# Performance work log

Measured on AMD Instinct MI355X. Metric: run time of the kernel, lower is better.

Reference implementation:

```python
import jax, jax.numpy as jnp
import numpy as np

N_IN = 200000   # input points/voxels
N_OUT = 100000  # output points (downconv transition)
E = 1600000     # neighbor-list entries (edges)
K = 9           # kernel_size: number of spatial filter bins
C_IN = 32
C_A = 24        # unnormalized branch channels (output_channels - normalized_channels)
C_B = 8         # importance-normalized branch channels


def setup_inputs() -> dict:
    key = jax.random.key(0)
    ks = jax.random.split(key, 8)
    feats = jax.random.normal(ks[0], (N_IN, C_IN), dtype=jnp.float32)
    importance = jax.random.uniform(ks[1], (N_IN,), dtype=jnp.float32)
    W_a = jax.random.normal(ks[2], (K, C_IN, C_A), dtype=jnp.float32) * 0.05
    b_a = jnp.zeros((C_A,), dtype=jnp.float32)
    W_b = jax.random.normal(ks[3], (K, C_IN, C_B), dtype=jnp.float32) * 0.05
    b_b = jnp.zeros((C_B,), dtype=jnp.float32)
    neighbors_index = jax.random.randint(ks[4], (E,), 0, N_IN, dtype=jnp.int32)
    neighbors_kernel_index = jax.random.randint(ks[5], (E,), 0, K, dtype=jnp.int32)
    neighbors_out_index = jnp.sort(jax.random.randint(ks[6], (E,), 0, N_OUT, dtype=jnp.int32))
    return {
        'feats': feats, 'importance': importance,
        'W_a': W_a, 'b_a': b_a, 'W_b': W_b, 'b_b': b_b,
        'neighbors_index': neighbors_index,
        'neighbors_kernel_index': neighbors_kernel_index,
        'neighbors_out_index': neighbors_out_index,
    }


def reference(feats, importance, W_a, b_a, W_b, b_b,
              neighbors_index, neighbors_kernel_index, neighbors_out_index):
    # Gather input features along the neighbor list: [E, C_IN]
    gathered = feats[neighbors_index]
    # Combined segment id = output point * K + kernel bin, so one segment_sum
    # accumulates per-(output-point, kernel-bin) feature sums: [N_OUT, K, C_IN]
    seg = neighbors_out_index * K + neighbors_kernel_index

    # --- conv1a: plain sparse conv (no normalization) ---
    Sa = jax.ops.segment_sum(gathered, seg, num_segments=N_OUT * K)
    Sa = Sa.reshape(N_OUT, K, C_IN)
    feats_a = jax.nn.relu(jnp.einsum('nkc,kcf->nf', Sa, W_a) + b_a)

    # --- conv1b: importance-weighted, normalized sparse conv ---
    imp_e = importance[neighbors_index]  # per-edge importance from input points
    Sb = jax.ops.segment_sum(gathered * imp_e[:, None], seg, num_segments=N_OUT * K)
    Sb = Sb.reshape(N_OUT, K, C_IN)
    out_imp = jax.ops.segment_sum(imp_e, neighbors_out_index, num_segments=N_OUT)
    denom = jnp.where(out_imp > 0, out_imp, 1.0)
    feats_b = jax.nn.relu(jnp.einsum('nkc,kcf->nf', Sb, W_b) / denom[:, None] + b_b)

    feats1 = jnp.concatenate([feats_a, feats_b], axis=-1)  # [N_OUT, C_A + C_B]
    return feats1, out_imp
```

## Files before the change

kernel.cpp:

```cpp
#include <hip/hip_runtime.h>
#include <hip/hip_bf16.h>

static constexpr int KC   = 9;
static constexpr int CIN  = 32;
static constexpr int CA   = 24;
static constexpr int CB   = 8;
static constexpr int COUT = 32;
static constexpr int KCC  = KC * CIN;
static constexpr int SPP  = 2 * KCC;

__global__ void prep(const int* __restrict__ oidx, const int* __restrict__ nidx,
                     const float* __restrict__ importance,
                     const float* __restrict__ Wa, const float* __restrict__ Wb,
                     int* __restrict__ rp, float* __restrict__ imp_e,
                     float* __restrict__ Wc, int E, int nout) {
    int e = blockIdx.x * blockDim.x + threadIdx.x;
    if (e < E) {
        int cur  = oidx[e];
        int prev = (e == 0) ? -1 : oidx[e - 1];
        for (int id = prev + 1; id <= cur; ++id) rp[id] = e;
        if (e == E - 1) {
            for (int id = cur + 1; id <= nout; ++id) rp[id] = E;
        }
        imp_e[e] = importance[nidx[e]];
        if (e < KCC * COUT) {
            int f  = e & (COUT - 1);
            int kc = e >> 5;
            Wc[e] = (f < CA) ? Wa[kc * CA + f] : Wb[kc * CB + (f - CA)];
        }
    }
}

#define ACC_ADD(Q, V)                              \
    do {                                           \
        if      ((Q) == 0) acc[0] += (V);          \
        else if ((Q) == 1) acc[1] += (V);          \
        else if ((Q) == 2) acc[2] += (V);          \
        else if ((Q) == 3) acc[3] += (V);          \
        else if ((Q) == 4) acc[4] += (V);          \
        else if ((Q) == 5) acc[5] += (V);          \
        else if ((Q) == 6) acc[6] += (V);          \
        else if ((Q) == 7) acc[7] += (V);          \
        else               acc[8] += (V);          \
    } while (0)

__device__ __forceinline__ float readlane_f(float v, int l) {
    return __uint_as_float(__builtin_amdgcn_readlane(__float_as_uint(v), l));
}

__global__ __launch_bounds__(256) void accum_y(
    const float* __restrict__ feats, const float* __restrict__ imp_e,
    const int* __restrict__ nidx, const int* __restrict__ nkidx,
    const int* __restrict__ rp,
    __hip_bfloat16* __restrict__ S, float* __restrict__ impAcc, int nout)
{
    const int lane = threadIdx.x & 63;
    const int c    = lane & 31;
    const int h    = lane >> 5;
    const int l4   = lane & 3;
    int gw = (blockIdx.x * 256 + threadIdx.x) >> 6;
    gw = __builtin_amdgcn_readfirstlane(gw);
    const int NW = (gridDim.x * 256) >> 6;

    for (int n = gw; n < nout; n += NW) {
        const int start = rp[n];
        const int end   = rp[n + 1];

        float acc[KC];
#pragma unroll
        for (int k = 0; k < KC; ++k) acc[k] = 0.f;
        float accImp = 0.f;

        for (int e = start; e < end; e += 4) {
            int em = e + l4;
            if (em > end - 1) em = end - 1;
            int   metaI = nidx[em];
            int   metaQ = nkidx[em];
            float metaM = imp_e[em];

            int q0 = __builtin_amdgcn_readlane(metaQ, 0);
            int q1 = __builtin_amdgcn_readlane(metaQ, 1);
            int q2 = __builtin_amdgcn_readlane(metaQ, 2);
            int q3 = __builtin_amdgcn_readlane(metaQ, 3);
            int i0 = __builtin_amdgcn_readlane(metaI, 0);
            int i1 = __builtin_amdgcn_readlane(metaI, 1);
            int i2 = __builtin_amdgcn_readlane(metaI, 2);
            int i3 = __builtin_amdgcn_readlane(metaI, 3);
            float m0 = readlane_f(metaM, 0);
            float m1 = readlane_f(metaM, 1);
            float m2 = readlane_f(metaM, 2);
            float m3 = readlane_f(metaM, 3);

            float f0 = feats[(size_t)i0 * CIN + c];
            float f1 = feats[(size_t)i1 * CIN + c];
            float f2 = feats[(size_t)i2 * CIN + c];
            float f3 = feats[(size_t)i3 * CIN + c];

            if (e + 1 >= end) { f1 = 0.f; m1 = 0.f; }
            if (e + 2 >= end) { f2 = 0.f; m2 = 0.f; }
            if (e + 3 >= end) { f3 = 0.f; m3 = 0.f; }
            accImp += (m0 + m1) + (m2 + m3);

            float v0 = f0 * (h ? m0 : 1.0f);
            float v1 = f1 * (h ? m1 : 1.0f);
            float v2 = f2 * (h ? m2 : 1.0f);
            float v3 = f3 * (h ? m3 : 1.0f);
            ACC_ADD(q0, v0);
            ACC_ADD(q1, v1);
            ACC_ADD(q2, v2);
            ACC_ADD(q3, v3);
        }

        __hip_bfloat16* Sp = S + (size_t)n * SPP + h * KCC + c;
#pragma unroll
        for (int k = 0; k < KC; ++k) Sp[k * CIN] = __float2bfloat16(acc[k]);
        if (lane == 0) impAcc[n] = accImp;
    }
}
#undef ACC_ADD

__global__ __launch_bounds__(256) void epilogue_g(
    const __hip_bfloat16* __restrict__ S, const float* __restrict__ impAcc,
    const float* __restrict__ Wc, const float* __restrict__ ba,
    const float* __restrict__ bb,
    float* __restrict__ outf, float* __restrict__ outimp, int nout)
{
    const int gtid   = blockIdx.x * 256 + threadIdx.x;
    const bool valid = (gtid < nout);
    const int n      = valid ? gtid : (nout - 1);

    const unsigned short* Sp =
        reinterpret_cast<const unsigned short*>(S + (size_t)n * SPP);

    float acc[COUT];
#pragma unroll
    for (int j = 0; j < COUT; ++j) acc[j] = 0.f;

    for (int t = 0; t < KCC; t += 8) {
        uint4 ua = *reinterpret_cast<const uint4*>(Sp + t);
        uint4 ub = *reinterpret_cast<const uint4*>(Sp + KCC + t);
        unsigned int uaw[4] = {ua.x, ua.y, ua.z, ua.w};
        unsigned int ubw[4] = {ub.x, ub.y, ub.z, ub.w};
        float sav[8], sbv[8];
#pragma unroll
        for (int p = 0; p < 4; ++p) {
            sav[2 * p]     = __uint_as_float(uaw[p] << 16);
            sav[2 * p + 1] = __uint_as_float(uaw[p] & 0xffff0000u);
            sbv[2 * p]     = __uint_as_float(ubw[p] << 16);
            sbv[2 * p + 1] = __uint_as_float(ubw[p] & 0xffff0000u);
        }
#pragma unroll
        for (int u = 0; u < 8; ++u) {
            const float* w = Wc + (t + u) * COUT;
#pragma unroll
            for (int j = 0; j < CA; ++j) acc[j] = fmaf(sav[u], w[j], acc[j]);
#pragma unroll
            for (int j = 0; j < CB; ++j)
                acc[CA + j] = fmaf(sbv[u], w[CA + j], acc[CA + j]);
        }
    }

    float impTot = impAcc[n];
    float denom  = impTot > 0.f ? impTot : 1.f;

    if (valid) {
        float res[COUT];
#pragma unroll
        for (int j = 0; j < CA; ++j) res[j] = fmaxf(acc[j] + ba[j], 0.f);
#pragma unroll
        for (int j = 0; j < CB; ++j)
            res[CA + j] = fmaxf(acc[CA + j] / denom + bb[j], 0.f);
        float4* op = reinterpret_cast<float4*>(outf + (size_t)n * COUT);
#pragma unroll
        for (int j4 = 0; j4 < 8; ++j4)
            op[j4] = make_float4(res[4 * j4], res[4 * j4 + 1],
                                 res[4 * j4 + 2], res[4 * j4 + 3]);
        outimp[n] = impTot;
    }
}

static constexpr int WSTR = KC * CIN + 4;
static constexpr int PPB = 16;
static constexpr int TPB = 512;
static constexpr int NHW = TPB / 32;

__global__ void build_rowptr_fb(const int* __restrict__ oidx, int* __restrict__ rp,
                                int E, int nout) {
    int e = blockIdx.x * blockDim.x + threadIdx.x;
    if (e >= E) return;
    int cur  = oidx[e];
    int prev = (e == 0) ? -1 : oidx[e - 1];
    for (int id = prev + 1; id <= cur; ++id) rp[id] = e;
    if (e == E - 1) {
        for (int id = cur + 1; id <= nout; ++id) rp[id] = E;
    }
}

__global__ void pack_weights_fkc(const float* __restrict__ Wa,
                                 const float* __restrict__ Wb,
                                 float* __restrict__ Wt) {
    int t = blockIdx.x * blockDim.x + threadIdx.x;
    if (t >= COUT * KC * CIN) return;
    int f = t / (KC * CIN);
    int r = t % (KC * CIN);
    Wt[t] = (f < CA) ? Wa[r * CA + f] : Wb[r * CB + (f - CA)];
}

__global__ __launch_bounds__(TPB) void fused_block(
    const float* __restrict__ feats, const float* __restrict__ importance,
    const float* __restrict__ Wt, const float* __restrict__ ba,
    const float* __restrict__ bb,
    const int* __restrict__ nidx, const int* __restrict__ nkidx,
    const int* __restrict__ noidx, const int* __restrict__ rp,
    float* __restrict__ outf, float* __restrict__ outimp, int nout)
{
    __shared__ __align__(16) float sW[COUT * WSTR];
    __shared__ __align__(16) float sS[PPB][2][KC * CIN];
    __shared__ float sImp[PPB];

    const int tid = threadIdx.x;
    const int hw  = tid >> 5;
    const int c   = tid & 31;
    const int p0  = blockIdx.x * PPB;

    {
        float* pS = &sS[0][0][0];
        for (int i = tid; i < PPB * 2 * KC * CIN; i += TPB) pS[i] = 0.f;
        for (int i = tid; i < COUT * KC * CIN; i += TPB) {
            int f = i / (KC * CIN);
            int r = i % (KC * CIN);
            sW[f * WSTR + r] = Wt[i];
        }
        if (tid < PPB) sImp[tid] = 0.f;
    }
    __syncthreads();

    const int pend   = (p0 + PPB < nout) ? (p0 + PPB) : nout;
    const int estart = rp[p0];
    const int eend   = rp[pend];
    const int cnt    = eend - estart;
    const int per    = (cnt + NHW - 1) / NHW;
    int a = estart + hw * per;
    int b = a + per; if (b > eend) b = eend;

    float* S0 = &sS[0][0][0];
    for (int e = a; e < b; ++e) {
        int   n0 = noidx[e], i0 = nidx[e], q0 = nkidx[e];
        float m0 = importance[i0];
        float f0 = feats[(size_t)i0 * CIN + c];
        float* bp = S0 + (n0 - p0) * (2 * KC * CIN) + q0 * CIN + c;
        atomicAdd(bp, f0);
        atomicAdd(bp + KC * CIN, f0 * m0);
        if (c == 0) atomicAdd(&sImp[n0 - p0], m0);
    }
    __syncthreads();

    const int wave = tid >> 6;
    const int lane = tid & 63;
    const int f    = lane & 31;
    const int h    = lane >> 5;
#pragma unroll
    for (int rep = 0; rep < 2; ++rep) {
        const int slot = wave * 2 + rep;
        const int n    = p0 + slot;
        if (n >= nout) break;
        float impTot = sImp[slot];
        float denom  = impTot > 0.f ? impTot : 1.f;
        const float* Sbase = &sS[slot][(f < CA) ? 0 : 1][0];
        const float* Wbase = sW + f * WSTR;
        float acc = 0.f;
#pragma unroll
        for (int k = 0; k < KC; ++k) {
            int off = k * CIN + h * 16;
#pragma unroll
            for (int j = 0; j < 16; ++j) acc = fmaf(Sbase[off + j], Wbase[off + j], acc);
        }
        float tot = acc + __shfl_xor(acc, 32, 64);
        if (h == 0) {
            float res = (f < CA) ? (tot + ba[f]) : (tot / denom + bb[f - CA]);
            outf[(size_t)n * COUT + f] = fmaxf(res, 0.f);
        }
        if (lane == 0) outimp[n] = impTot;
    }
}

extern "C" void kernel_launch(void* const* d_in, const int* in_sizes, int n_in,
                              void* d_out, int out_size, void* d_ws, size_t ws_size,
                              hipStream_t stream) {
    const float* feats      = (const float*)d_in[0];
    const float* importance = (const float*)d_in[1];
    const float* Wa         = (const float*)d_in[2];
    const float* ba         = (const float*)d_in[3];
    const float* Wb         = (const float*)d_in[4];
    const float* bb         = (const float*)d_in[5];
    const int*   nidx       = (const int*)d_in[6];
    const int*   nkidx      = (const int*)d_in[7];
    const int*   noidx      = (const int*)d_in[8];

    const int E    = in_sizes[6];
    const int nout = out_size / (COUT + 1);

    float* outf   = (float*)d_out;
    float* outimp = outf + (size_t)nout * COUT;

    const size_t off_imp = ((size_t)nout * SPP * sizeof(__hip_bfloat16) + 255) & ~(size_t)255;
    const size_t off_wc  = (off_imp + (size_t)nout * sizeof(float) + 255) & ~(size_t)255;
    const size_t off_rp  = (off_wc + (size_t)KCC * COUT * sizeof(float) + 255) & ~(size_t)255;
    const size_t off_ie  = (off_rp + (size_t)(nout + 1) * sizeof(int) + 255) & ~(size_t)255;
    const size_t need    = off_ie + (size_t)E * sizeof(float);

    if (ws_size >= need) {
        __hip_bfloat16* S = (__hip_bfloat16*)d_ws;
        float* impAcc = (float*)((char*)d_ws + off_imp);
        float* Wc     = (float*)((char*)d_ws + off_wc);
        int*   rp     = (int*)((char*)d_ws + off_rp);
        float* imp_e  = (float*)((char*)d_ws + off_ie);

        prep<<<(E + 255) / 256, 256, 0, stream>>>(
            noidx, nidx, importance, Wa, Wb, rp, imp_e, Wc, E, nout);
        accum_y<<<2048, 256, 0, stream>>>(
            feats, imp_e, nidx, nkidx, rp, S, impAcc, nout);
        epilogue_g<<<(nout + 255) / 256, 256, 0, stream>>>(
            S, impAcc, Wc, ba, bb, outf, outimp, nout);
    } else {
        int*   rp = (int*)d_ws;
        size_t rp_bytes = ((size_t)(nout + 1) * sizeof(int) + 255) & ~(size_t)255;
        float* Wt = (float*)((char*)d_ws + rp_bytes);

        build_rowptr_fb<<<(E + 255) / 256, 256, 0, stream>>>(noidx, rp, E, nout);
        pack_weights_fkc<<<(COUT * KC * CIN + 255) / 256, 256, 0, stream>>>(Wa, Wb, Wt);
        fused_block<<<(nout + PPB - 1) / PPB, TPB, 0, stream>>>(
            feats, importance, Wt, ba, bb, nidx, nkidx, noidx, rp,
            outf, outimp, nout);
    }
}
```

Measured before the change: 132.7 us.

## Pack neighbor index and kernel bin into one key and process 8 edges per step

The prep kernel now packs each edge's input index and kernel bin into a single int key, so the accumulation kernel loads one metadata word per edge instead of two. The accumulation loop processes 8 edges per iteration instead of 4, which exposes more independent feature gathers in flight. The importance sum is computed per lane and reduced with shuffles. The epilogue block size also drops from 256 to 128. The cost is an extra E-sized workspace array plus its write in prep, more registers per thread in the accumulation loop, and an index packing that assumes the input index fits in 28 bits.

```diff
diff --git a/kernel.cpp b/kernel.cpp
--- a/kernel.cpp
+++ b/kernel.cpp
@@ -10,10 +10,12 @@
 static constexpr int SPP  = 2 * KCC;
 
 __global__ void prep(const int* __restrict__ oidx, const int* __restrict__ nidx,
+                     const int* __restrict__ nkidx,
                      const float* __restrict__ importance,
                      const float* __restrict__ Wa, const float* __restrict__ Wb,
                      int* __restrict__ rp, float* __restrict__ imp_e,
-                     float* __restrict__ Wc, int E, int nout) {
+                     int* __restrict__ keym, float* __restrict__ Wc,
+                     int E, int nout) {
     int e = blockIdx.x * blockDim.x + threadIdx.x;
     if (e < E) {
         int cur  = oidx[e];
@@ -22,7 +24,9 @@
         if (e == E - 1) {
             for (int id = cur + 1; id <= nout; ++id) rp[id] = E;
         }
-        imp_e[e] = importance[nidx[e]];
+        int i = nidx[e];
+        imp_e[e] = importance[i];
+        keym[e]  = (i << 4) | nkidx[e];
         if (e < KCC * COUT) {
             int f  = e & (COUT - 1);
             int kc = e >> 5;
@@ -48,16 +52,22 @@
     return __uint_as_float(__builtin_amdgcn_readlane(__float_as_uint(v), l));
 }
 
-__global__ __launch_bounds__(256) void accum_y(
+#define EDGE(J)                                                        \
+    do {                                                               \
+        float fz = f##J * o##J;                                        \
+        float mm = h ? m##J : 1.0f;    \
+        ACC_ADD(q##J, fz * mm);                                        \
+    } while (0)
+
+__global__ __launch_bounds__(256) void accum_z(
     const float* __restrict__ feats, const float* __restrict__ imp_e,
-    const int* __restrict__ nidx, const int* __restrict__ nkidx,
-    const int* __restrict__ rp,
+    const int* __restrict__ keym, const int* __restrict__ rp,
     __hip_bfloat16* __restrict__ S, float* __restrict__ impAcc, int nout)
 {
     const int lane = threadIdx.x & 63;
     const int c    = lane & 31;
     const int h    = lane >> 5;
-    const int l4   = lane & 3;
+    const int l8   = lane & 7;
     int gw = (blockIdx.x * 256 + threadIdx.x) >> 6;
     gw = __builtin_amdgcn_readfirstlane(gw);
     const int NW = (gridDim.x * 256) >> 6;
@@ -69,63 +79,80 @@
         float acc[KC];
 #pragma unroll
         for (int k = 0; k < KC; ++k) acc[k] = 0.f;
-        float accImp = 0.f;
-
-        for (int e = start; e < end; e += 4) {
-            int em = e + l4;
+        float accImpL = 0.f;
+
+        for (int e = start; e < end; e += 8) {
+            int em = e + l8;
             if (em > end - 1) em = end - 1;
-            int   metaI = nidx[em];
-            int   metaQ = nkidx[em];
-            float metaM = imp_e[em];
-
-            int q0 = __builtin_amdgcn_readlane(metaQ, 0);
-            int q1 = __builtin_amdgcn_readlane(metaQ, 1);
-            int q2 = __builtin_amdgcn_readlane(metaQ, 2);
-            int q3 = __builtin_amdgcn_readlane(metaQ, 3);
-            int i0 = __builtin_amdgcn_readlane(metaI, 0);
-            int i1 = __builtin_amdgcn_readlane(metaI, 1);
-            int i2 = __builtin_amdgcn_readlane(metaI, 2);
-            int i3 = __builtin_amdgcn_readlane(metaI, 3);
-            float m0 = readlane_f(metaM, 0);
-            float m1 = readlane_f(metaM, 1);
-            float m2 = readlane_f(metaM, 2);
-            float m3 = readlane_f(metaM, 3);
+            int   keyv = keym[em];
+            float mv   = imp_e[em];
+
+            accImpL += (e + l8 < end) ? mv : 0.f;
+
+            int k0 = __builtin_amdgcn_readlane(keyv, 0);
+            int k1 = __builtin_amdgcn_readlane(keyv, 1);
+            int k2 = __builtin_amdgcn_readlane(keyv, 2);
+            int k3 = __builtin_amdgcn_readlane(keyv, 3);
+            int k4 = __builtin_amdgcn_readlane(keyv, 4);
+            int k5 = __builtin_amdgcn_readlane(keyv, 5);
+            int k6 = __builtin_amdgcn_readlane(keyv, 6);
+            int k7 = __builtin_amdgcn_readlane(keyv, 7);
+            float m0 = readlane_f(mv, 0), m1 = readlane_f(mv, 1);
+            float m2 = readlane_f(mv, 2), m3 = readlane_f(mv, 3);
+            float m4 = readlane_f(mv, 4), m5 = readlane_f(mv, 5);
+            float m6 = readlane_f(mv, 6), m7 = readlane_f(mv, 7);
+            int i0 = k0 >> 4, q0 = k0 & 15;
+            int i1 = k1 >> 4, q1 = k1 & 15;
+            int i2 = k2 >> 4, q2 = k2 & 15;
+            int i3 = k3 >> 4, q3 = k3 & 15;
+            int i4 = k4 >> 4, q4 = k4 & 15;
+            int i5 = k5 >> 4, q5 = k5 & 15;
+            int i6 = k6 >> 4, q6 = k6 & 15;
+            int i7 = k7 >> 4, q7 = k7 & 15;
+
+            const float o0 = 1.0f;
+            float o1 = (e + 1 < end) ? 1.0f : 0.0f;
+            float o2 = (e + 2 < end) ? 1.0f : 0.0f;
+            float o3 = (e + 3 < end) ? 1.0f : 0.0f;
+            float o4 = (e + 4 < end) ? 1.0f : 0.0f;
+            float o5 = (e + 5 < end) ? 1.0f : 0.0f;
+            float o6 = (e + 6 < end) ? 1.0f : 0.0f;
+            float o7 = (e + 7 < end) ? 1.0f : 0.0f;
 
             float f0 = feats[(size_t)i0 * CIN + c];
             float f1 = feats[(size_t)i1 * CIN + c];
             float f2 = feats[(size_t)i2 * CIN + c];
             float f3 = feats[(size_t)i3 * CIN + c];
-
-            if (e + 1 >= end) { f1 = 0.f; m1 = 0.f; }
-            if (e + 2 >= end) { f2 = 0.f; m2 = 0.f; }
-            if (e + 3 >= end) { f3 = 0.f; m3 = 0.f; }
-            accImp += (m0 + m1) + (m2 + m3);
-
-            float v0 = f0 * (h ? m0 : 1.0f);
-            float v1 = f1 * (h ? m1 : 1.0f);
-            float v2 = f2 * (h ? m2 : 1.0f);
-            float v3 = f3 * (h ? m3 : 1.0f);
-            ACC_ADD(q0, v0);
-            ACC_ADD(q1, v1);
-            ACC_ADD(q2, v2);
-            ACC_ADD(q3, v3);
-        }
+            float f4 = feats[(size_t)i4 * CIN + c];
+            float f5 = feats[(size_t)i5 * CIN + c];
+            float f6 = feats[(size_t)i6 * CIN + c];
+            float f7 = feats[(size_t)i7 * CIN + c];
+
+            EDGE(0); EDGE(1); EDGE(2); EDGE(3);
+            EDGE(4); EDGE(5); EDGE(6); EDGE(7);
+        }
+
+        float impTot = accImpL;
+        impTot += __shfl_xor(impTot, 1, 64);
+        impTot += __shfl_xor(impTot, 2, 64);
+        impTot += __shfl_xor(impTot, 4, 64);
 
         __hip_bfloat16* Sp = S + (size_t)n * SPP + h * KCC + c;
 #pragma unroll
         for (int k = 0; k < KC; ++k) Sp[k * CIN] = __float2bfloat16(acc[k]);
-        if (lane == 0) impAcc[n] = accImp;
-    }
-}
+        if (lane == 0) impAcc[n] = impTot;
+    }
+}
+#undef EDGE
 #undef ACC_ADD
 
-__global__ __launch_bounds__(256) void epilogue_g(
+__global__ __launch_bounds__(128) void epilogue_g(
     const __hip_bfloat16* __restrict__ S, const float* __restrict__ impAcc,
     const float* __restrict__ Wc, const float* __restrict__ ba,
     const float* __restrict__ bb,
     float* __restrict__ outf, float* __restrict__ outimp, int nout)
 {
-    const int gtid   = blockIdx.x * 256 + threadIdx.x;
+    const int gtid   = blockIdx.x * 128 + threadIdx.x;
     const bool valid = (gtid < nout);
     const int n      = valid ? gtid : (nout - 1);
 
@@ -307,7 +334,8 @@
     const size_t off_wc  = (off_imp + (size_t)nout * sizeof(float) + 255) & ~(size_t)255;
     const size_t off_rp  = (off_wc + (size_t)KCC * COUT * sizeof(float) + 255) & ~(size_t)255;
     const size_t off_ie  = (off_rp + (size_t)(nout + 1) * sizeof(int) + 255) & ~(size_t)255;
-    const size_t need    = off_ie + (size_t)E * sizeof(float);
+    const size_t off_km  = (off_ie + (size_t)E * sizeof(float) + 255) & ~(size_t)255;
+    const size_t need    = off_km + (size_t)E * sizeof(int);
 
     if (ws_size >= need) {
         __hip_bfloat16* S = (__hip_bfloat16*)d_ws;
@@ -315,12 +343,13 @@
         float* Wc     = (float*)((char*)d_ws + off_wc);
         int*   rp     = (int*)((char*)d_ws + off_rp);
         float* imp_e  = (float*)((char*)d_ws + off_ie);
+        int*   keym   = (int*)((char*)d_ws + off_km);
 
         prep<<<(E + 255) / 256, 256, 0, stream>>>(
-            noidx, nidx, importance, Wa, Wb, rp, imp_e, Wc, E, nout);
-        accum_y<<<2048, 256, 0, stream>>>(
-            feats, imp_e, nidx, nkidx, rp, S, impAcc, nout);
-        epilogue_g<<<(nout + 255) / 256, 256, 0, stream>>>(
+            noidx, nidx, nkidx, importance, Wa, Wb, rp, imp_e, keym, Wc, E, nout);
+        accum_z<<<2048, 256, 0, stream>>>(
+            feats, imp_e, keym, rp, S, impAcc, nout);
+        epilogue_g<<<(nout + 127) / 128, 128, 0, stream>>>(
             S, impAcc, Wc, ba, bb, outf, outimp, nout);
     } else {
         int*   rp = (int*)d_ws;
```

New measurement: 139.0 us. 1.05x slower.
